# Performance work log

Hardware: AMD Instinct MI355X
Metric: run time of the kernel (lower is better)

## Reference

```python
import jax, jax.numpy as jnp
import numpy as np

HALF = 32          # (input_dim-1)//2
HIDDEN = 128
OUT_DIM = 10
B, T, C = 256, 512, 65


def setup_inputs() -> dict:
    key = jax.random.key(0)
    ks = jax.random.split(key, 20)
    s = 0.05
    gin = HALF + HIDDEN
    inp = {
        "times": jnp.arange(T, dtype=jnp.float32),
        "coeff_a": jax.random.normal(ks[0], (B, T - 1, C), jnp.float32),
        "coeff_b": jax.random.normal(ks[1], (B, T - 1, C), jnp.float32),
        "coeff_two_c": jax.random.normal(ks[2], (B, T - 1, C), jnp.float32),
        "coeff_three_d": jax.random.normal(ks[3], (B, T - 1, C), jnp.float32),
        "final_index": jax.random.randint(ks[4], (B,), 0, T),
        "Wr": jax.random.normal(ks[5], (gin, HIDDEN), jnp.float32) * s,
        "br": jnp.zeros((HIDDEN,), jnp.float32),
        "Wz": jax.random.normal(ks[6], (gin, HIDDEN), jnp.float32) * s,
        "bz": jnp.zeros((HIDDEN,), jnp.float32),
        "Wxn": jax.random.normal(ks[7], (HALF, HIDDEN), jnp.float32) * s,
        "bxn": jnp.zeros((HIDDEN,), jnp.float32),
        "Whn": jax.random.normal(ks[8], (HIDDEN, HIDDEN), jnp.float32) * s,
        "bhn": jnp.zeros((HIDDEN,), jnp.float32),
        "W_ode": jax.random.normal(ks[9], (HIDDEN, HIDDEN), jnp.float32) * s,
        "b_ode": jnp.zeros((HIDDEN,), jnp.float32),
        "W_lin": jax.random.normal(ks[10], (HIDDEN, OUT_DIM), jnp.float32) * s,
        "b_lin": jnp.zeros((OUT_DIM,), jnp.float32),
    }
    return inp


def _forward(times, coeff_a, coeff_b, coeff_two_c, coeff_three_d, final_index,
             Wr, br, Wz, bz, Wxn, bxn, Whn, bhn, W_ode, b_ode, W_lin, b_lin):
    maxlen = coeff_b.shape[-2] - 1

    def eval_spline(t):
        idx = jnp.clip(jnp.sum(t > times) - 1, 0, maxlen)
        fr = t - times[idx]
        inner = 0.5 * coeff_two_c[:, idx, :] + coeff_three_d[:, idx, :] * (fr / 3.0)
        inner = coeff_b[:, idx, :] + inner * fr
        return coeff_a[:, idx, :] + inner * fr  # [B, C]

    X = jax.vmap(eval_spline, out_axes=1)(times)  # [B, T, C]
    # difference the observation-indicator channels over time; make channel 0 a time delta
    X = X.at[:, 1:, 1:1 + HALF].add(-X[:, :-1, 1:1 + HALF])
    X = X.at[:, 0, 0].add(-times[0])
    X = X.at[:, 1:, 0].add(-times[:-1])

    nbatch = X.shape[0]

    def gru(x, h):
        comb = jnp.concatenate([x, h], axis=1)
        r = jax.nn.sigmoid(comb @ Wr + br)
        z = jax.nn.sigmoid(comb @ Wz + bz)
        n = jnp.tanh(x @ Wxn + bxn + (h @ Whn + bhn) * r)
        return (1.0 - z) * n + z * h

    def f_ode(h):
        return jnp.tanh(h @ W_ode + b_ode)

    def evolve(h, td):
        # single RK4 step from 0 to td
        k1 = f_ode(h)
        k2 = f_ode(h + 0.5 * td * k1)
        k3 = f_ode(h + 0.5 * td * k2)
        k4 = f_ode(h + td * k3)
        return h + (td / 6.0) * (k1 + 2.0 * k2 + 2.0 * k3 + k4)

    def step(h, dt, Xi):
        obs = jnp.max(Xi[:, 1:1 + HALF], axis=1) > 0.5
        Xp = Xi[:, 1 + HALF:].at[:, 0].add(dt)
        new_h = gru(Xp, h)

        def take(hd):
            h0, dt0 = hd
            return (jnp.where(obs[:, None], new_h, h0),
                    dt0 + jnp.where(obs, 0.0, Xi[:, 0]))

        return jax.lax.cond(jnp.any(obs), take, lambda hd: hd, (h, dt))

    z0 = jnp.zeros((nbatch, HIDDEN), X.dtype)
    dt0 = jnp.zeros((nbatch,), X.dtype)
    h0, dt0 = step(z0, dt0, X[:, 0])

    time_diffs = times[1:] - times[:-1]
    Xs = jnp.moveaxis(X[:, 1:], 1, 0)  # [T-1, B, C]

    def scan_body(carry, inp):
        h, dt = carry
        td, Xi = inp
        h = evolve(h, td)
        h, dt = step(h, dt, Xi)
        return (h, dt), h

    _, hs_rest = jax.lax.scan(scan_body, (h0, dt0), (time_diffs, Xs))
    out = jnp.concatenate([h0[:, None], jnp.moveaxis(hs_rest, 0, 1)], axis=1)  # [B, T, H]
    final = out[jnp.arange(nbatch), final_index]  # [B, H]
    return final @ W_lin + b_lin


def reference(times, coeff_a, coeff_b, coeff_two_c, coeff_three_d, final_index,
              Wr, br, Wz, bz, Wxn, bxn, Whn, bhn, W_ode, b_ode, W_lin, b_lin):
    return _forward(times, coeff_a, coeff_b, coeff_two_c, coeff_three_d, final_index,
                    Wr, br, Wz, bz, Wxn, bxn, Whn, bhn, W_ode, b_ode, W_lin, b_lin)
```

## Files before the change

kernel.cpp:

```cpp
#include <hip/hip_runtime.h>
#include <string.h>

#define TT 512
#define BB 256
#define CC 65
#define HALFC 32
#define HID 128
#define ODIM 10

typedef _Float16 half2_t __attribute__((ext_vector_type(2)));

__device__ __forceinline__ float ftanh(float x) {
  float u = __builtin_amdgcn_exp2f(x * -2.885390082f);
  return fmaf(2.f, __builtin_amdgcn_rcpf(1.f + u), -1.f);
}
__device__ __forceinline__ float fsig(float x) {
  float u = __builtin_amdgcn_exp2f(x * -1.442695041f);
  return __builtin_amdgcn_rcpf(1.f + u);
}

__device__ __forceinline__ half2_t h2cvt(float a, float b) {
  auto r = __builtin_amdgcn_cvt_pkrtz(a, b);
  half2_t o;
  memcpy(&o, &r, sizeof(o));
  return o;
}

__device__ __forceinline__ float fdot2h(half2_t a, half2_t b, float c) {
#if __has_builtin(__builtin_amdgcn_fdot2)
  return __builtin_amdgcn_fdot2(a, b, c, false);
#else
  float d;
  asm("v_dot2_f32_f16 %0, %1, %2, %3" : "=v"(d) : "v"(a), "v"(b), "v"(c));
  return d;
#endif
}

template <int CTRL>
__device__ __forceinline__ float dpp_add(float x) {
  return x + __int_as_float(__builtin_amdgcn_update_dpp(
      0, __float_as_int(x), CTRL, 0xF, 0xF, true));
}
__device__ __forceinline__ float red8(float x) {
  x = dpp_add<0x101>(x);
  x = dpp_add<0x102>(x);
  x = dpp_add<0x104>(x);
  return x;
}

__device__ __forceinline__ void block_sync_lds() {
  asm volatile("s_waitcnt lgkmcnt(0)" ::: "memory");
  __builtin_amdgcn_s_barrier();
  asm volatile("" ::: "memory");
}
__device__ __forceinline__ void vm_wait0() {
  asm volatile("s_waitcnt vmcnt(0)" ::: "memory");
}

__device__ __forceinline__ int h2_slot_byteoff(int s) {
  const int c = s >> 2;
  const int p = ((c & 1) << 3) | (c >> 1);
  return p * 16 + (s & 3) * 4;
}

__global__ void prep0(const float* __restrict__ times, float4* __restrict__ si,
                      int* __restrict__ anyobs) {
  __shared__ float ts[TT];
  int t = threadIdx.x;
  ts[t] = times[t];
  __syncthreads();
  float tv = ts[t];
  int cnt = 0;
  for (int jj = 0; jj < TT; ++jj) cnt += (tv > ts[jj]) ? 1 : 0;
  int idx = cnt - 1;
  idx = min(max(idx, 0), TT - 2);
  float4 o;
  o.x = __int_as_float(idx);
  o.y = tv - ts[idx];
  o.z = (t == 0) ? 0.f : (tv - ts[t - 1]);
  o.w = (t == 0) ? ts[0] : ts[t - 1];
  si[t] = o;
  anyobs[t] = 0;
}

__global__ void prep_obs(const float* __restrict__ ca, const float* __restrict__ cb,
                         const float* __restrict__ cc2, const float* __restrict__ cd,
                         const float4* __restrict__ si, int* __restrict__ anyobs,
                         unsigned char* __restrict__ obs) {
  int grp = blockIdx.x * (blockDim.x >> 5) + (threadIdx.x >> 5);
  int lane = threadIdx.x & 31;
  int t = grp & (TT - 1);
  int b = grp / TT;
  int ch = 1 + lane;
  float4 s = si[t];
  int idx = __float_as_int(s.x);
  float fr = s.y;
  size_t base = ((size_t)b * (TT - 1) + idx) * CC + ch;
  float f3 = fr / 3.f;
  float v = ca[base] + (cb[base] + (0.5f * cc2[base] + cd[base] * f3) * fr) * fr;
  float D = v;
  if (t >= 1) {
    float4 sp = si[t - 1];
    int idxp = __float_as_int(sp.x);
    float frp = sp.y;
    size_t basep = ((size_t)b * (TT - 1) + idxp) * CC + ch;
    float f3p = frp / 3.f;
    float vp = ca[basep] + (cb[basep] + (0.5f * cc2[basep] + cd[basep] * f3p) * frp) * frp;
    D = v - vp;
  }
  float m = D;
  #pragma unroll
  for (int off = 16; off >= 1; off >>= 1) m = fmaxf(m, __shfl_xor(m, off));
  if (lane == 0) {
    unsigned char o = (m > 0.5f) ? (unsigned char)1 : (unsigned char)0;
    obs[(size_t)b * TT + t] = o;
    if (o) atomicOr(&anyobs[t], 1);
  }
}

__launch_bounds__(512, 1)
__global__ void ode_main(
    const float* __restrict__ ca, const float* __restrict__ cb,
    const float* __restrict__ cc2, const float* __restrict__ cd,
    const int* __restrict__ final_index,
    const float* __restrict__ Wr, const float* __restrict__ br,
    const float* __restrict__ Wz, const float* __restrict__ bz,
    const float* __restrict__ Wxn, const float* __restrict__ bxn,
    const float* __restrict__ Whn, const float* __restrict__ bhn,
    const float* __restrict__ Wode, const float* __restrict__ bode,
    const float* __restrict__ Wlin, const float* __restrict__ blin,
    const float4* __restrict__ si, const int* __restrict__ anyobs,
    const unsigned char* __restrict__ obsArr,
    float* __restrict__ out)
{
  __shared__ alignas(16) half2_t hS2[HID / 2];
  __shared__ alignas(16) half2_t vA2[HID / 2];
  __shared__ alignas(16) half2_t vB2[HID / 2];
  __shared__ alignas(16) float xs[HALFC];
  __shared__ alignas(16) float4 siL[TT];
  __shared__ unsigned char flagL[TT];

  const int tid = threadIdx.x;
  const int b = blockIdx.x;
  const int lane = tid & 63;
  const int wv = tid >> 6;
  const int jslot = lane >> 3;
  const int kk = lane & 7;
  const int j0 = wv * 16 + jslot * 2;
  const int spair = wv * 8 + jslot;
  const int wroff = h2_slot_byteoff(spair);

  half2_t wodeH[16], whnH[16], wrhH[16], wzhH[16];
  #pragma unroll
  for (int i = 0; i < 8; ++i) {
    const int r0 = 16 * kk + 2 * i, r1 = r0 + 1;
    float2 q0, q1;
    q0 = *(const float2*)&Wode[r0 * HID + j0];
    q1 = *(const float2*)&Wode[r1 * HID + j0];
    wodeH[2*i]   = h2cvt(q0.x, q1.x);
    wodeH[2*i+1] = h2cvt(q0.y, q1.y);
    q0 = *(const float2*)&Whn[r0 * HID + j0];
    q1 = *(const float2*)&Whn[r1 * HID + j0];
    whnH[2*i]   = h2cvt(q0.x, q1.x);
    whnH[2*i+1] = h2cvt(q0.y, q1.y);
    q0 = *(const float2*)&Wr[(HALFC + r0) * HID + j0];
    q1 = *(const float2*)&Wr[(HALFC + r1) * HID + j0];
    wrhH[2*i]   = h2cvt(q0.x, q1.x);
    wrhH[2*i+1] = h2cvt(q0.y, q1.y);
    q0 = *(const float2*)&Wz[(HALFC + r0) * HID + j0];
    q1 = *(const float2*)&Wz[(HALFC + r1) * HID + j0];
    wzhH[2*i]   = h2cvt(q0.x, q1.x);
    wzhH[2*i+1] = h2cvt(q0.y, q1.y);
  }
  float wrx[8], wzx[8], wxn[8];
  #pragma unroll
  for (int i = 0; i < 4; ++i) {
    const int xrow = 4 * kk + i;
    float2 q;
    q = *(const float2*)&Wr [xrow * HID + j0]; wrx[2*i] = q.x; wrx[2*i+1] = q.y;
    q = *(const float2*)&Wz [xrow * HID + j0]; wzx[2*i] = q.x; wzx[2*i+1] = q.y;
    q = *(const float2*)&Wxn[xrow * HID + j0]; wxn[2*i] = q.x; wxn[2*i+1] = q.y;
  }
  float bo0, bo1, bh0, bh1, br0, br1, bz0, bz1, bx0, bx1;
  { float2 q;
    q = *(const float2*)&bode[j0]; bo0 = q.x; bo1 = q.y;
    q = *(const float2*)&bhn [j0]; bh0 = q.x; bh1 = q.y;
    q = *(const float2*)&br  [j0]; br0 = q.x; br1 = q.y;
    q = *(const float2*)&bz  [j0]; bz0 = q.x; bz1 = q.y;
    q = *(const float2*)&bxn [j0]; bx0 = q.x; bx1 = q.y;
  }
  const int fidx = final_index[b];

  {
    siL[tid] = si[tid];
    const int ao = anyobs[tid];
    const unsigned char o = obsArr[(size_t)b * TT + tid];
    flagL[tid] = (unsigned char)((ao ? 1 : 0) | (o ? 2 : 0));
  }
  if (tid < HID / 2) {
    const half2_t z2 = {(_Float16)0.f, (_Float16)0.f};
    hS2[tid] = z2; vA2[tid] = z2; vB2[tid] = z2;
  }
  if (tid < HALFC) xs[tid] = 0.f;
  float hj0 = 0.f, hj1 = 0.f;
  float dtv = 0.f;
  block_sync_lds();

  auto mv = [&](const half2_t* __restrict__ buf, const half2_t (&w)[16],
                float& o0, float& o1) {
    half2_t v2[8];
    #pragma unroll
    for (int i = 0; i < 4; ++i) {
      v2[i]     = buf[4 * kk + i];
      v2[4 + i] = buf[32 + 4 * kk + i];
    }
    float a0 = 0.f, a1 = 0.f, b0 = 0.f, b1 = 0.f;
    #pragma unroll
    for (int i = 0; i < 4; ++i) {
      a0 = fdot2h(v2[i],     w[2*i],       a0);
      a1 = fdot2h(v2[i],     w[2*i+1],     a1);
      b0 = fdot2h(v2[4 + i], w[2*(4+i)],   b0);
      b1 = fdot2h(v2[4 + i], w[2*(4+i)+1], b1);
    }
    o0 = red8(a0 + b0);
    o1 = red8(a1 + b1);
  };

  float4 s = siL[0];
  int flg = flagL[0];

  for (int t = 0; ; ++t) {
    const int sidx = __float_as_int(s.x);
    const float fr = s.y, td = s.z, tsub = s.w;
    const bool apply = (flg & 1) && (flg & 2);

    float xa = 0.f, xb = 0.f, xc = 0.f, xd = 0.f;
    float ya = 0.f, yb = 0.f, yc = 0.f, yd = 0.f;
    if (tid < 32) {
      const size_t base = ((size_t)b * (TT - 1) + sidx) * CC;
      const int ch = 33 + tid;
      xa = ca[base + ch]; xb = cb[base + ch]; xc = cc2[base + ch]; xd = cd[base + ch];
      if (tid == 0) { ya = ca[base]; yb = cb[base]; yc = cc2[base]; yd = cd[base]; }
    }

    if (t > 0) {
      const float htd = 0.5f * td;
      float p0, p1, k0, k1, ks0, ks1;
      mv(hS2, wodeH, p0, p1);
      k0 = ftanh(p0 + bo0); k1 = ftanh(p1 + bo1);
      ks0 = k0; ks1 = k1;
      if (kk == 0)
        *(half2_t*)((char*)vA2 + wroff) =
            h2cvt(fmaf(htd, k0, hj0), fmaf(htd, k1, hj1));
      block_sync_lds();
      mv(vA2, wodeH, p0, p1);
      k0 = ftanh(p0 + bo0); k1 = ftanh(p1 + bo1);
      ks0 = fmaf(2.f, k0, ks0); ks1 = fmaf(2.f, k1, ks1);
      if (kk == 0)
        *(half2_t*)((char*)vB2 + wroff) =
            h2cvt(fmaf(htd, k0, hj0), fmaf(htd, k1, hj1));
      block_sync_lds();
      mv(vB2, wodeH, p0, p1);
      k0 = ftanh(p0 + bo0); k1 = ftanh(p1 + bo1);
      ks0 = fmaf(2.f, k0, ks0); ks1 = fmaf(2.f, k1, ks1);
      if (kk == 0)
        *(half2_t*)((char*)vA2 + wroff) =
            h2cvt(fmaf(td, k0, hj0), fmaf(td, k1, hj1));
      block_sync_lds();
      mv(vA2, wodeH, p0, p1);
      k0 = ftanh(p0 + bo0); k1 = ftanh(p1 + bo1);
      ks0 += k0; ks1 += k1;
      hj0 = fmaf(td * (1.f / 6.f), ks0, hj0);
      hj1 = fmaf(td * (1.f / 6.f), ks1, hj1);
      if (kk == 0)
        *(half2_t*)((char*)vB2 + wroff) = h2cvt(hj0, hj1);
    }

    float xdelta = 0.f;
    vm_wait0();
    if (tid < 32) {
      const float f3 = fr * (1.f / 3.f);
      float sv = xa + (xb + (0.5f * xc + xd * f3) * fr) * fr;
      if (tid == 0) {
        const float s0 = ya + (yb + (0.5f * yc + yd * f3) * fr) * fr;
        xdelta = s0 - tsub;
        sv += dtv;
      }
      xs[tid] = sv;
    }
    block_sync_lds();

    {
      half2_t v2[8];
      #pragma unroll
      for (int i = 0; i < 4; ++i) {
        v2[i]     = vB2[4 * kk + i];
        v2[4 + i] = vB2[32 + 4 * kk + i];
      }
      float rp0 = 0.f, rp1 = 0.f, zp0 = 0.f, zp1 = 0.f, gp0 = 0.f, gp1 = 0.f;
      #pragma unroll
      for (int i = 0; i < 8; ++i) {
        rp0 = fdot2h(v2[i], wrhH[2*i],   rp0);
        rp1 = fdot2h(v2[i], wrhH[2*i+1], rp1);
        zp0 = fdot2h(v2[i], wzhH[2*i],   zp0);
        zp1 = fdot2h(v2[i], wzhH[2*i+1], zp1);
        gp0 = fdot2h(v2[i], whnH[2*i],   gp0);
        gp1 = fdot2h(v2[i], whnH[2*i+1], gp1);
      }
      float xp0 = 0.f, xp1 = 0.f;
      const float4 xq = ((const float4*)xs)[kk];
      const float xv[4] = {xq.x, xq.y, xq.z, xq.w};
      #pragma unroll
      for (int i = 0; i < 4; ++i) {
        rp0 = fmaf(xv[i], wrx[2*i],   rp0); rp1 = fmaf(xv[i], wrx[2*i+1], rp1);
        zp0 = fmaf(xv[i], wzx[2*i],   zp0); zp1 = fmaf(xv[i], wzx[2*i+1], zp1);
        xp0 = fmaf(xv[i], wxn[2*i],   xp0); xp1 = fmaf(xv[i], wxn[2*i+1], xp1);
      }
      rp0 = red8(rp0); rp1 = red8(rp1);
      zp0 = red8(zp0); zp1 = red8(zp1);
      gp0 = red8(gp0); gp1 = red8(gp1);
      xp0 = red8(xp0); xp1 = red8(xp1);
      const float r0 = fsig(rp0 + br0), r1 = fsig(rp1 + br1);
      const float z0 = fsig(zp0 + bz0), z1 = fsig(zp1 + bz1);
      const float n0 = ftanh(xp0 + bx0 + (gp0 + bh0) * r0);
      const float n1 = ftanh(xp1 + bx1 + (gp1 + bh1) * r1);
      const float h0n = fmaf(z0, hj0 - n0, n0);
      const float h1n = fmaf(z1, hj1 - n1, n1);
      hj0 = apply ? h0n : hj0;
      hj1 = apply ? h1n : hj1;
      if (kk == 0)
        *(half2_t*)((char*)hS2 + wroff) = h2cvt(hj0, hj1);
    }
    if (tid == 0 && (flg & 1) && !(flg & 2)) dtv += xdelta;

    if (t == fidx) break;
    const int tn = t + 1;
    s = siL[tn];
    flg = flagL[tn];
    block_sync_lds();
  }

  block_sync_lds();
  if (tid < ODIM) {
    float acc = blin[tid];
    const _Float16* hf = (const _Float16*)hS2;
    #pragma unroll 8
    for (int q = 0; q < HID; ++q) {
      const int cq = q >> 3;
      const int p = ((cq & 1) << 3) | (cq >> 1);
      const float hv = (float)hf[p * 8 + (q & 7)];
      acc = fmaf(hv, Wlin[q * ODIM + tid], acc);
    }
    out[b * ODIM + tid] = acc;
  }
}

extern "C" void kernel_launch(void* const* d_in, const int* in_sizes, int n_in,
                              void* d_out, int out_size, void* d_ws, size_t ws_size,
                              hipStream_t stream) {
  const float* times = (const float*)d_in[0];
  const float* ca   = (const float*)d_in[1];
  const float* cb   = (const float*)d_in[2];
  const float* cc2  = (const float*)d_in[3];
  const float* cd   = (const float*)d_in[4];
  const int*   fidx = (const int*)d_in[5];
  const float* Wr   = (const float*)d_in[6];
  const float* br   = (const float*)d_in[7];
  const float* Wz   = (const float*)d_in[8];
  const float* bz   = (const float*)d_in[9];
  const float* Wxn  = (const float*)d_in[10];
  const float* bxn  = (const float*)d_in[11];
  const float* Whn  = (const float*)d_in[12];
  const float* bhn  = (const float*)d_in[13];
  const float* Wode = (const float*)d_in[14];
  const float* bode = (const float*)d_in[15];
  const float* Wlin = (const float*)d_in[16];
  const float* blin = (const float*)d_in[17];
  float* out = (float*)d_out;

  char* ws = (char*)d_ws;
  float4* si = (float4*)ws;
  int* anyobs = (int*)(ws + TT * 16);
  unsigned char* obs = (unsigned char*)(ws + TT * 16 + TT * 4);

  prep0<<<1, TT, 0, stream>>>(times, si, anyobs);
  prep_obs<<<(BB * TT) / 8, 256, 0, stream>>>(ca, cb, cc2, cd, si, anyobs, obs);
  ode_main<<<BB, 512, 0, stream>>>(ca, cb, cc2, cd, fidx, Wr, br, Wz, bz,
                                   Wxn, bxn, Whn, bhn, Wode, bode, Wlin, blin,
                                   si, anyobs, obs, out);
}
```

Before: 1.044 ms.

## Halve block size and split each hidden-pair matvec over four lanes

The ODE/GRU kernel now uses 256 threads per block instead of 512. Each output pair is reduced over 4 lanes with 32 weight half2 registers per matrix, replacing 8 lanes with 16, so the DPP reduction is one step shorter. LDS reads become contiguous 16-byte half8 loads in place of the swizzled layout. The input-projection weights move to fp16 dot2, with channel 0 kept in fp32 as a separate FMA. The aim is to cut barrier cost and per-step latency in the sequential recurrence, at the price of doubled register pressure and more fp16 rounding of the inputs.

After: 956.8 us. 8.3% less time.

```diff
diff --git a/kernel.cpp b/kernel.cpp
--- a/kernel.cpp
+++ b/kernel.cpp
@@ -9,6 +9,7 @@
 #define ODIM 10
 
 typedef _Float16 half2_t __attribute__((ext_vector_type(2)));
+typedef _Float16 half8_t __attribute__((ext_vector_type(8)));
 
 __device__ __forceinline__ float ftanh(float x) {
   float u = __builtin_amdgcn_exp2f(x * -2.885390082f);
@@ -27,13 +28,7 @@
 }
 
 __device__ __forceinline__ float fdot2h(half2_t a, half2_t b, float c) {
-#if __has_builtin(__builtin_amdgcn_fdot2)
   return __builtin_amdgcn_fdot2(a, b, c, false);
-#else
-  float d;
-  asm("v_dot2_f32_f16 %0, %1, %2, %3" : "=v"(d) : "v"(a), "v"(b), "v"(c));
-  return d;
-#endif
 }
 
 template <int CTRL>
@@ -41,10 +36,9 @@
   return x + __int_as_float(__builtin_amdgcn_update_dpp(
       0, __float_as_int(x), CTRL, 0xF, 0xF, true));
 }
-__device__ __forceinline__ float red8(float x) {
+__device__ __forceinline__ float red4(float x) {
   x = dpp_add<0x101>(x);
   x = dpp_add<0x102>(x);
-  x = dpp_add<0x104>(x);
   return x;
 }
 
@@ -55,12 +49,6 @@
 }
 __device__ __forceinline__ void vm_wait0() {
   asm volatile("s_waitcnt vmcnt(0)" ::: "memory");
-}
-
-__device__ __forceinline__ int h2_slot_byteoff(int s) {
-  const int c = s >> 2;
-  const int p = ((c & 1) << 3) | (c >> 1);
-  return p * 16 + (s & 3) * 4;
 }
 
 __global__ void prep0(const float* __restrict__ times, float4* __restrict__ si,
@@ -118,7 +106,7 @@
   }
 }
 
-__launch_bounds__(512, 1)
+__launch_bounds__(256, 1)
 __global__ void ode_main(
     const float* __restrict__ ca, const float* __restrict__ cb,
     const float* __restrict__ cc2, const float* __restrict__ cd,
@@ -136,7 +124,8 @@
   __shared__ alignas(16) half2_t hS2[HID / 2];
   __shared__ alignas(16) half2_t vA2[HID / 2];
   __shared__ alignas(16) half2_t vB2[HID / 2];
-  __shared__ alignas(16) float xs[HALFC];
+  __shared__ alignas(16) _Float16 xh[HALFC];
+  __shared__ float xs0f;
   __shared__ alignas(16) float4 siL[TT];
   __shared__ unsigned char flagL[TT];
 
@@ -144,42 +133,53 @@
   const int b = blockIdx.x;
   const int lane = tid & 63;
   const int wv = tid >> 6;
-  const int jslot = lane >> 3;
-  const int kk = lane & 7;
-  const int j0 = wv * 16 + jslot * 2;
-  const int spair = wv * 8 + jslot;
-  const int wroff = h2_slot_byteoff(spair);
-
-  half2_t wodeH[16], whnH[16], wrhH[16], wzhH[16];
+  const int p = lane >> 2;
+  const int kk = lane & 3;
+  const int s = wv * 16 + p;
+  const int j0 = 2 * s;
+  const int wbyte = 4 * s;
+
+  half2_t wodeH[32], whnH[32], wrhH[32], wzhH[32];
   #pragma unroll
-  for (int i = 0; i < 8; ++i) {
-    const int r0 = 16 * kk + 2 * i, r1 = r0 + 1;
+  for (int i = 0; i < 16; ++i) {
+    const int r0 = 32 * kk + 2 * i, r1 = r0 + 1;
     float2 q0, q1;
     q0 = *(const float2*)&Wode[r0 * HID + j0];
     q1 = *(const float2*)&Wode[r1 * HID + j0];
-    wodeH[2*i]   = h2cvt(q0.x, q1.x);
-    wodeH[2*i+1] = h2cvt(q0.y, q1.y);
+    wodeH[2*i] = h2cvt(q0.x, q1.x); wodeH[2*i+1] = h2cvt(q0.y, q1.y);
     q0 = *(const float2*)&Whn[r0 * HID + j0];
     q1 = *(const float2*)&Whn[r1 * HID + j0];
-    whnH[2*i]   = h2cvt(q0.x, q1.x);
-    whnH[2*i+1] = h2cvt(q0.y, q1.y);
+    whnH[2*i] = h2cvt(q0.x, q1.x); whnH[2*i+1] = h2cvt(q0.y, q1.y);
     q0 = *(const float2*)&Wr[(HALFC + r0) * HID + j0];
     q1 = *(const float2*)&Wr[(HALFC + r1) * HID + j0];
-    wrhH[2*i]   = h2cvt(q0.x, q1.x);
-    wrhH[2*i+1] = h2cvt(q0.y, q1.y);
+    wrhH[2*i] = h2cvt(q0.x, q1.x); wrhH[2*i+1] = h2cvt(q0.y, q1.y);
     q0 = *(const float2*)&Wz[(HALFC + r0) * HID + j0];
     q1 = *(const float2*)&Wz[(HALFC + r1) * HID + j0];
-    wzhH[2*i]   = h2cvt(q0.x, q1.x);
-    wzhH[2*i+1] = h2cvt(q0.y, q1.y);
-  }
-  float wrx[8], wzx[8], wxn[8];
+    wzhH[2*i] = h2cvt(q0.x, q1.x); wzhH[2*i+1] = h2cvt(q0.y, q1.y);
+  }
+  half2_t wrxH[8], wzxH[8], wxnH[8];
   #pragma unroll
   for (int i = 0; i < 4; ++i) {
-    const int xrow = 4 * kk + i;
-    float2 q;
-    q = *(const float2*)&Wr [xrow * HID + j0]; wrx[2*i] = q.x; wrx[2*i+1] = q.y;
-    q = *(const float2*)&Wz [xrow * HID + j0]; wzx[2*i] = q.x; wzx[2*i+1] = q.y;
-    q = *(const float2*)&Wxn[xrow * HID + j0]; wxn[2*i] = q.x; wxn[2*i+1] = q.y;
+    const int c0 = 8 * kk + 2 * i, c1 = c0 + 1;
+    float2 q0, q1;
+    q0 = *(const float2*)&Wr[c0 * HID + j0];
+    q1 = *(const float2*)&Wr[c1 * HID + j0];
+    wrxH[i] = h2cvt(q0.x, q1.x); wrxH[4+i] = h2cvt(q0.y, q1.y);
+    q0 = *(const float2*)&Wz[c0 * HID + j0];
+    q1 = *(const float2*)&Wz[c1 * HID + j0];
+    wzxH[i] = h2cvt(q0.x, q1.x); wzxH[4+i] = h2cvt(q0.y, q1.y);
+    q0 = *(const float2*)&Wxn[c0 * HID + j0];
+    q1 = *(const float2*)&Wxn[c1 * HID + j0];
+    wxnH[i] = h2cvt(q0.x, q1.x); wxnH[4+i] = h2cvt(q0.y, q1.y);
+  }
+  float wr0a = 0.f, wr0b = 0.f, wz0a = 0.f, wz0b = 0.f, wx0a = 0.f, wx0b = 0.f;
+  if (kk == 0) {
+    wrxH[0][0] = (_Float16)0.f; wrxH[4][0] = (_Float16)0.f;
+    wzxH[0][0] = (_Float16)0.f; wzxH[4][0] = (_Float16)0.f;
+    wxnH[0][0] = (_Float16)0.f; wxnH[4][0] = (_Float16)0.f;
+    wr0a = Wr[j0];  wr0b = Wr[j0 + 1];
+    wz0a = Wz[j0];  wz0b = Wz[j0 + 1];
+    wx0a = Wxn[j0]; wx0b = Wxn[j0 + 1];
   }
   float bo0, bo1, bh0, bh1, br0, br1, bz0, bz1, bx0, bx1;
   { float2 q;
@@ -191,54 +191,62 @@
   }
   const int fidx = final_index[b];
 
-  {
-    siL[tid] = si[tid];
-    const int ao = anyobs[tid];
-    const unsigned char o = obsArr[(size_t)b * TT + tid];
-    flagL[tid] = (unsigned char)((ao ? 1 : 0) | (o ? 2 : 0));
+  #pragma unroll
+  for (int it = 0; it < 2; ++it) {
+    const int tt = tid + it * 256;
+    siL[tt] = si[tt];
+    const int ao = anyobs[tt];
+    const unsigned char o = obsArr[(size_t)b * TT + tt];
+    flagL[tt] = (unsigned char)((ao ? 1 : 0) | (o ? 2 : 0));
   }
   if (tid < HID / 2) {
     const half2_t z2 = {(_Float16)0.f, (_Float16)0.f};
     hS2[tid] = z2; vA2[tid] = z2; vB2[tid] = z2;
   }
-  if (tid < HALFC) xs[tid] = 0.f;
+  if (tid < HALFC) xh[tid] = (_Float16)0.f;
+  if (tid == 0) xs0f = 0.f;
   float hj0 = 0.f, hj1 = 0.f;
   float dtv = 0.f;
   block_sync_lds();
 
-  auto mv = [&](const half2_t* __restrict__ buf, const half2_t (&w)[16],
+  auto mv = [&](const half2_t* __restrict__ buf, const half2_t (&w)[32],
                 float& o0, float& o1) {
-    half2_t v2[8];
+    half2_t v2[16];
     #pragma unroll
-    for (int i = 0; i < 4; ++i) {
-      v2[i]     = buf[4 * kk + i];
-      v2[4 + i] = buf[32 + 4 * kk + i];
+    for (int q = 0; q < 4; ++q) {
+      const half8_t x8 = *(const half8_t*)((const char*)buf + 64 * kk + 16 * q);
+      v2[4*q+0] = __builtin_shufflevector(x8, x8, 0, 1);
+      v2[4*q+1] = __builtin_shufflevector(x8, x8, 2, 3);
+      v2[4*q+2] = __builtin_shufflevector(x8, x8, 4, 5);
+      v2[4*q+3] = __builtin_shufflevector(x8, x8, 6, 7);
     }
     float a0 = 0.f, a1 = 0.f, b0 = 0.f, b1 = 0.f;
     #pragma unroll
-    for (int i = 0; i < 4; ++i) {
+    for (int i = 0; i < 8; ++i) {
       a0 = fdot2h(v2[i],     w[2*i],       a0);
       a1 = fdot2h(v2[i],     w[2*i+1],     a1);
-      b0 = fdot2h(v2[4 + i], w[2*(4+i)],   b0);
-      b1 = fdot2h(v2[4 + i], w[2*(4+i)+1], b1);
-    }
-    o0 = red8(a0 + b0);
-    o1 = red8(a1 + b1);
+      b0 = fdot2h(v2[8 + i], w[2*(8+i)],   b0);
+      b1 = fdot2h(v2[8 + i], w[2*(8+i)+1], b1);
+    }
+    o0 = red4(a0 + b0);
+    o1 = red4(a1 + b1);
   };
 
-  float4 s = siL[0];
+  float4 sv4 = siL[0];
   int flg = flagL[0];
 
   for (int t = 0; ; ++t) {
-    const int sidx = __float_as_int(s.x);
-    const float fr = s.y, td = s.z, tsub = s.w;
+    const int sidx = __float_as_int(sv4.x);
+    const float fr = sv4.y, td = sv4.z, tsub = sv4.w;
     const bool apply = (flg & 1) && (flg & 2);
 
+    const int xch = wv * 8 + lane;
+    const bool xlane = (lane < 8);
     float xa = 0.f, xb = 0.f, xc = 0.f, xd = 0.f;
     float ya = 0.f, yb = 0.f, yc = 0.f, yd = 0.f;
-    if (tid < 32) {
+    if (xlane) {
       const size_t base = ((size_t)b * (TT - 1) + sidx) * CC;
-      const int ch = 33 + tid;
+      const int ch = 33 + xch;
       xa = ca[base + ch]; xb = cb[base + ch]; xc = cc2[base + ch]; xd = cd[base + ch];
       if (tid == 0) { ya = ca[base]; yb = cb[base]; yc = cc2[base]; yd = cd[base]; }
     }
@@ -250,21 +258,21 @@
       k0 = ftanh(p0 + bo0); k1 = ftanh(p1 + bo1);
       ks0 = k0; ks1 = k1;
       if (kk == 0)
-        *(half2_t*)((char*)vA2 + wroff) =
+        *(half2_t*)((char*)vA2 + wbyte) =
             h2cvt(fmaf(htd, k0, hj0), fmaf(htd, k1, hj1));
       block_sync_lds();
       mv(vA2, wodeH, p0, p1);
       k0 = ftanh(p0 + bo0); k1 = ftanh(p1 + bo1);
       ks0 = fmaf(2.f, k0, ks0); ks1 = fmaf(2.f, k1, ks1);
       if (kk == 0)
-        *(half2_t*)((char*)vB2 + wroff) =
+        *(half2_t*)((char*)vB2 + wbyte) =
             h2cvt(fmaf(htd, k0, hj0), fmaf(htd, k1, hj1));
       block_sync_lds();
       mv(vB2, wodeH, p0, p1);
       k0 = ftanh(p0 + bo0); k1 = ftanh(p1 + bo1);
       ks0 = fmaf(2.f, k0, ks0); ks1 = fmaf(2.f, k1, ks1);
       if (kk == 0)
-        *(half2_t*)((char*)vA2 + wroff) =
+        *(half2_t*)((char*)vA2 + wbyte) =
             h2cvt(fmaf(td, k0, hj0), fmaf(td, k1, hj1));
       block_sync_lds();
       mv(vA2, wodeH, p0, p1);
@@ -273,33 +281,37 @@
       hj0 = fmaf(td * (1.f / 6.f), ks0, hj0);
       hj1 = fmaf(td * (1.f / 6.f), ks1, hj1);
       if (kk == 0)
-        *(half2_t*)((char*)vB2 + wroff) = h2cvt(hj0, hj1);
+        *(half2_t*)((char*)vB2 + wbyte) = h2cvt(hj0, hj1);
     }
 
     float xdelta = 0.f;
     vm_wait0();
-    if (tid < 32) {
+    if (xlane) {
       const float f3 = fr * (1.f / 3.f);
       float sv = xa + (xb + (0.5f * xc + xd * f3) * fr) * fr;
       if (tid == 0) {
         const float s0 = ya + (yb + (0.5f * yc + yd * f3) * fr) * fr;
         xdelta = s0 - tsub;
         sv += dtv;
+        xs0f = sv;
       }
-      xs[tid] = sv;
+      xh[xch] = (_Float16)sv;
     }
     block_sync_lds();
 
     {
-      half2_t v2[8];
+      half2_t v2[16];
       #pragma unroll
-      for (int i = 0; i < 4; ++i) {
-        v2[i]     = vB2[4 * kk + i];
-        v2[4 + i] = vB2[32 + 4 * kk + i];
+      for (int q = 0; q < 4; ++q) {
+        const half8_t x8 = *(const half8_t*)((const char*)vB2 + 64 * kk + 16 * q);
+        v2[4*q+0] = __builtin_shufflevector(x8, x8, 0, 1);
+        v2[4*q+1] = __builtin_shufflevector(x8, x8, 2, 3);
+        v2[4*q+2] = __builtin_shufflevector(x8, x8, 4, 5);
+        v2[4*q+3] = __builtin_shufflevector(x8, x8, 6, 7);
       }
       float rp0 = 0.f, rp1 = 0.f, zp0 = 0.f, zp1 = 0.f, gp0 = 0.f, gp1 = 0.f;
       #pragma unroll
-      for (int i = 0; i < 8; ++i) {
+      for (int i = 0; i < 16; ++i) {
         rp0 = fdot2h(v2[i], wrhH[2*i],   rp0);
         rp1 = fdot2h(v2[i], wrhH[2*i+1], rp1);
         zp0 = fdot2h(v2[i], wzhH[2*i],   zp0);
@@ -308,18 +320,33 @@
         gp1 = fdot2h(v2[i], whnH[2*i+1], gp1);
       }
       float xp0 = 0.f, xp1 = 0.f;
-      const float4 xq = ((const float4*)xs)[kk];
-      const float xv[4] = {xq.x, xq.y, xq.z, xq.w};
-      #pragma unroll
-      for (int i = 0; i < 4; ++i) {
-        rp0 = fmaf(xv[i], wrx[2*i],   rp0); rp1 = fmaf(xv[i], wrx[2*i+1], rp1);
-        zp0 = fmaf(xv[i], wzx[2*i],   zp0); zp1 = fmaf(xv[i], wzx[2*i+1], zp1);
-        xp0 = fmaf(xv[i], wxn[2*i],   xp0); xp1 = fmaf(xv[i], wxn[2*i+1], xp1);
+      {
+        const half8_t x8 = *(const half8_t*)((const char*)xh + 16 * kk);
+        half2_t xv2[4];
+        xv2[0] = __builtin_shufflevector(x8, x8, 0, 1);
+        xv2[1] = __builtin_shufflevector(x8, x8, 2, 3);
+        xv2[2] = __builtin_shufflevector(x8, x8, 4, 5);
+        xv2[3] = __builtin_shufflevector(x8, x8, 6, 7);
+        #pragma unroll
+        for (int i = 0; i < 4; ++i) {
+          rp0 = fdot2h(xv2[i], wrxH[i],   rp0);
+          rp1 = fdot2h(xv2[i], wrxH[4+i], rp1);
+          zp0 = fdot2h(xv2[i], wzxH[i],   zp0);
+          zp1 = fdot2h(xv2[i], wzxH[4+i], zp1);
+          xp0 = fdot2h(xv2[i], wxnH[i],   xp0);
+          xp1 = fdot2h(xv2[i], wxnH[4+i], xp1);
+        }
       }
-      rp0 = red8(rp0); rp1 = red8(rp1);
-      zp0 = red8(zp0); zp1 = red8(zp1);
-      gp0 = red8(gp0); gp1 = red8(gp1);
-      xp0 = red8(xp0); xp1 = red8(xp1);
+      if (kk == 0) {
+        const float x0 = xs0f;
+        rp0 = fmaf(x0, wr0a, rp0); rp1 = fmaf(x0, wr0b, rp1);
+        zp0 = fmaf(x0, wz0a, zp0); zp1 = fmaf(x0, wz0b, zp1);
+        xp0 = fmaf(x0, wx0a, xp0); xp1 = fmaf(x0, wx0b, xp1);
+      }
+      rp0 = red4(rp0); rp1 = red4(rp1);
+      zp0 = red4(zp0); zp1 = red4(zp1);
+      gp0 = red4(gp0); gp1 = red4(gp1);
+      xp0 = red4(xp0); xp1 = red4(xp1);
       const float r0 = fsig(rp0 + br0), r1 = fsig(rp1 + br1);
       const float z0 = fsig(zp0 + bz0), z1 = fsig(zp1 + bz1);
       const float n0 = ftanh(xp0 + bx0 + (gp0 + bh0) * r0);
@@ -329,13 +356,13 @@
       hj0 = apply ? h0n : hj0;
       hj1 = apply ? h1n : hj1;
       if (kk == 0)
-        *(half2_t*)((char*)hS2 + wroff) = h2cvt(hj0, hj1);
+        *(half2_t*)((char*)hS2 + wbyte) = h2cvt(hj0, hj1);
     }
     if (tid == 0 && (flg & 1) && !(flg & 2)) dtv += xdelta;
 
     if (t == fidx) break;
     const int tn = t + 1;
-    s = siL[tn];
+    sv4 = siL[tn];
     flg = flagL[tn];
     block_sync_lds();
   }
@@ -346,9 +373,7 @@
     const _Float16* hf = (const _Float16*)hS2;
     #pragma unroll 8
     for (int q = 0; q < HID; ++q) {
-      const int cq = q >> 3;
-      const int p = ((cq & 1) << 3) | (cq >> 1);
-      const float hv = (float)hf[p * 8 + (q & 7)];
+      const float hv = (float)hf[q];
       acc = fmaf(hv, Wlin[q * ODIM + tid], acc);
     }
     out[b * ODIM + tid] = acc;
@@ -385,7 +410,7 @@
 
   prep0<<<1, TT, 0, stream>>>(times, si, anyobs);
   prep_obs<<<(BB * TT) / 8, 256, 0, stream>>>(ca, cb, cc2, cd, si, anyobs, obs);
-  ode_main<<<BB, 512, 0, stream>>>(ca, cb, cc2, cd, fidx, Wr, br, Wz, bz,
+  ode_main<<<BB, 256, 0, stream>>>(ca, cb, cc2, cd, fidx, Wr, br, Wz, bz,
                                    Wxn, bxn, Whn, bhn, Wode, bode, Wlin, blin,
                                    si, anyobs, obs, out);
 }
```
